# Kernel tuning notes

Measured on AMD Instinct MI355X. Metric: run time of the kernel, lower is better.

## Reference

```python
import jax, jax.numpy as jnp
import numpy as np

N_NODES = 50000
N_EDGES = 800000
IN_DIM = 128
HID_DIM = 256
N_CLASS = 40
PROP_STEP = 3
DROPOUT = 0.0  # eval-mode drop_node scale = (1 - DROPOUT)


def setup_inputs() -> dict:
    key = jax.random.key(0)
    k = jax.random.split(key, 6)
    features = jax.random.normal(k[0], (N_NODES, IN_DIM), dtype=jnp.float32)
    src = jax.random.randint(k[1], (N_EDGES,), 0, N_NODES)
    dst = jax.random.randint(k[2], (N_EDGES,), 0, N_NODES)
    W1 = jax.random.normal(k[3], (IN_DIM, HID_DIM), dtype=jnp.float32) / np.sqrt(IN_DIM)
    b1 = jnp.zeros((HID_DIM,), dtype=jnp.float32)
    W2 = jax.random.normal(k[4], (HID_DIM, N_CLASS), dtype=jnp.float32) / np.sqrt(HID_DIM)
    b2 = jnp.zeros((N_CLASS,), dtype=jnp.float32)
    return {"features": features, "src": src, "dst": dst,
            "W1": W1, "b1": b1, "W2": W2, "b2": b2}


def reference(features, src, dst, W1, b1, W2, b2):
    N = features.shape[0]
    # in-degree-based symmetric normalization: norm = deg^{-1/2}, deg clamped to >= 1
    degs = jax.ops.segment_sum(jnp.ones_like(dst, dtype=jnp.float32), dst,
                               num_segments=N)
    norm = jnp.clip(degs, 1.0, None) ** -0.5              # [N]
    w = norm[src] * norm[dst]                             # [E] edge weights (u_mul_v)

    # eval-mode drop_node: scale features by (1 - drop_rate)
    x = features * (1.0 - DROPOUT)
    y = x
    for _ in range(PROP_STEP):
        # u_mul_e: gather source features, scale by edge weight, scatter-sum to dst
        m = x[src] * w[:, None]                           # [E, F]
        x = jax.ops.segment_sum(m, dst, num_segments=N)   # [N, F]
        y = y + x
    feat = y / (PROP_STEP + 1)

    # MLP (use_bn=False, dropouts are 0 / eval): relu(linear) -> linear
    h = jax.nn.relu(feat @ W1 + b1)
    logits = h @ W2 + b2
    return jax.nn.log_softmax(logits, axis=-1)
```

## Files before the change

kernel.cpp:

```cpp
#include <hip/hip_runtime.h>

#define IN_DIM 128
#define HID    256
#define NCLS   40
#define BSHIFT 8
#define BSZ    256
#define MAXNB  256
#define CHUNK  4096
#define CAP    5120

static inline size_t align256(size_t x) { return (x + 255) & ~(size_t)255; }

typedef __attribute__((ext_vector_type(2))) float f32x2;

__device__ inline unsigned pack_bf16x2(float x, float y) {
    unsigned xb = __float_as_uint(x), yb = __float_as_uint(y);
    unsigned lo = (xb + 0x7fffu + ((xb >> 16) & 1u)) >> 16;
    unsigned hi = (yb + 0x7fffu + ((yb >> 16) & 1u)) >> 16;
    return lo | (hi << 16);
}
__device__ inline unsigned short f2bf(float x) {
    unsigned b = __float_as_uint(x);
    return (unsigned short)((b + 0x7fffu + ((b >> 16) & 1u)) >> 16);
}

__device__ inline unsigned pack_fp8x4(float a, float b, float c, float d) {
    int v = __builtin_amdgcn_cvt_pk_fp8_f32(a, b, 0, false);
    v = __builtin_amdgcn_cvt_pk_fp8_f32(c, d, v, true);
    return (unsigned)v;
}

__global__ __launch_bounds__(256) void init_cursor_kernel(int* __restrict__ cursor) {
    cursor[threadIdx.x] = threadIdx.x * CAP;
}

__global__ __launch_bounds__(256) void bucket_scatter_kernel(
        const int* __restrict__ src, const int* __restrict__ dst,
        int* __restrict__ bucketCursor, int2* __restrict__ ebuf, int E) {
    __shared__ int hist[MAXNB], lofs[MAXNB], lcur[MAXNB], gbase[MAXNB];
    __shared__ int2 bin[CHUNK];
    int t = threadIdx.x, lane = t & 63, wave = t >> 6;
    int start = blockIdx.x * CHUNK;
    int cnt = min(CHUNK, E - start);
    hist[t] = 0;
    __syncthreads();
    for (int i = t; i < cnt; i += 256) atomicAdd(&hist[dst[start + i] >> BSHIFT], 1);
    __syncthreads();
    int v = hist[t];
    int s = v;
    for (int off = 1; off < 64; off <<= 1) {
        int u = __shfl_up(s, off, 64);
        if (lane >= off) s += u;
    }
    __shared__ int wsum[4];
    if (lane == 63) wsum[wave] = s;
    __syncthreads();
    if (t == 0) {
        int c = 0;
        for (int i = 0; i < 4; ++i) { int x = wsum[i]; wsum[i] = c; c += x; }
    }
    __syncthreads();
    int excl = wsum[wave] + s - v;
    lofs[t] = excl; lcur[t] = excl;
    if (v) gbase[t] = atomicAdd(&bucketCursor[t], v);
    __syncthreads();
    for (int i = t; i < cnt; i += 256) {
        int s0 = src[start + i], d0 = dst[start + i];
        int r = atomicAdd(&lcur[d0 >> BSHIFT], 1);
        bin[r] = make_int2(s0, d0);
    }
    __syncthreads();
    for (int i = t; i < cnt; i += 256) {
        int2 e = bin[i];
        int b = e.y >> BSHIFT;
        ebuf[gbase[b] + i - lofs[b]] = e;
    }
}

__global__ __launch_bounds__(256) void build_norm_kernel(
        const int2* __restrict__ ebuf, const int* __restrict__ bucketCursor,
        int* __restrict__ offs, int* __restrict__ degs, float* __restrict__ norm, int N) {
    __shared__ int hist[BSZ];
    __shared__ int wsum[4];
    int b = blockIdx.x, t = threadIdx.x, lane = t & 63, wave = t >> 6;
    int base = b * CAP;
    int cnt = bucketCursor[b] - base;
    hist[t] = 0;
    __syncthreads();
    for (int i = t; i < cnt; i += 256) atomicAdd(&hist[ebuf[base + i].y & (BSZ - 1)], 1);
    __syncthreads();
    int v = hist[t];
    int s = v;
    for (int off = 1; off < 64; off <<= 1) {
        int u = __shfl_up(s, off, 64);
        if (lane >= off) s += u;
    }
    if (lane == 63) wsum[wave] = s;
    __syncthreads();
    if (t == 0) {
        int c = 0;
        for (int i = 0; i < 4; ++i) { int x = wsum[i]; wsum[i] = c; c += x; }
    }
    __syncthreads();
    int excl = wsum[wave] + s - v;
    int node = b * BSZ + t;
    if (node < N) {
        offs[node] = base + excl;
        degs[node] = v;
        norm[node] = rsqrtf((float)(v > 0 ? v : 1));
    }
}

__global__ __launch_bounds__(256) void build_csr_kernel(
        const int2* __restrict__ ebuf, const int* __restrict__ bucketCursor,
        const int* __restrict__ offs, const float* __restrict__ norm,
        int2* __restrict__ csr, int N) {
    __shared__ int lcur[BSZ];
    __shared__ float snorm[BSZ];
    int b = blockIdx.x, t = threadIdx.x;
    int base = b * CAP;
    int cnt = bucketCursor[b] - base;
    int node = b * BSZ + t;
    lcur[t] = (node < N) ? offs[node] : 0;
    snorm[t] = (node < N) ? norm[node] : 0.f;
    __syncthreads();
    for (int i = t; i < cnt; i += 256) {
        int2 e = ebuf[base + i];
        int li = e.y & (BSZ - 1);
        float w = norm[e.x] * snorm[li];
        int p = atomicAdd(&lcur[li], 1);
        csr[p] = make_int2(e.x, __float_as_int(w));
    }
}

__global__ void prep_kernel(const float* __restrict__ feat, unsigned* __restrict__ x0,
                            const float* __restrict__ W1, const float* __restrict__ W2,
                            unsigned short* __restrict__ W1T, unsigned short* __restrict__ W2T,
                            int nfeat_dw) {
    int i = blockIdx.x * blockDim.x + threadIdx.x;
    if (i < nfeat_dw) {
        float4 f = *(const float4*)(feat + (size_t)i * 4);
        x0[i] = pack_fp8x4(f.x, f.y, f.z, f.w);
        return;
    }
    int j = i - nfeat_dw;
    if (j < 256 * 128) {
        int n = j >> 7, k = j & 127;
        W1T[j] = f2bf(W1[k * 256 + n]);
        return;
    }
    int k2 = j - 256 * 128;
    if (k2 < 48 * 256) {
        int c = k2 >> 8, kk = k2 & 255;
        W2T[k2] = (c < 40) ? f2bf(W2[kk * 40 + c]) : (unsigned short)0;
    }
}

#define ACCP16(dd, ww)                                                        \
    {                                                                         \
        f32x2 wv2 = {(ww), (ww)};                                             \
        c0 += __builtin_amdgcn_cvt_pk_f32_fp8((int)(dd).x, false) * wv2;      \
        c1 += __builtin_amdgcn_cvt_pk_f32_fp8((int)(dd).x, true ) * wv2;      \
        c2 += __builtin_amdgcn_cvt_pk_f32_fp8((int)(dd).y, false) * wv2;      \
        c3 += __builtin_amdgcn_cvt_pk_f32_fp8((int)(dd).y, true ) * wv2;      \
        c4 += __builtin_amdgcn_cvt_pk_f32_fp8((int)(dd).z, false) * wv2;      \
        c5 += __builtin_amdgcn_cvt_pk_f32_fp8((int)(dd).z, true ) * wv2;      \
        c6 += __builtin_amdgcn_cvt_pk_f32_fp8((int)(dd).w, false) * wv2;      \
        c7 += __builtin_amdgcn_cvt_pk_f32_fp8((int)(dd).w, true ) * wv2;      \
    }

#define RED2(a) { a += __shfl_xor(a, 8, 64); a += __shfl_xor(a, 16, 64); }

__global__ __launch_bounds__(256) void prop_kernel(
        const unsigned* __restrict__ xin, unsigned* __restrict__ xout,
        const int* __restrict__ offs, const int* __restrict__ degs,
        const int2* __restrict__ csr, int N) {
    int t = threadIdx.x;
    int wv = t >> 6, lane = t & 63;
    int h = lane >> 5, hl = lane & 31;
    int g = hl >> 3, gl = hl & 7;
    int v = blockIdx.x * 8 + wv * 2 + h;
    if (v >= N) return;
    __shared__ int2 sIW[4][2][32];
    int start = offs[v], end = start + degs[v];
    f32x2 c0 = {0.f,0.f}, c1 = {0.f,0.f}, c2 = {0.f,0.f}, c3 = {0.f,0.f};
    f32x2 c4 = {0.f,0.f}, c5 = {0.f,0.f}, c6 = {0.f,0.f}, c7 = {0.f,0.f};
    for (int k = start; k < end; k += 32) {
        int cnt = min(32, end - k);
        if (hl < cnt) sIW[wv][h][hl] = csr[k + hl];
        int j = 0;
        for (; j + 16 <= cnt; j += 16) {
            uint4 d[4]; float w[4];
#pragma unroll
            for (int u = 0; u < 4; ++u) {
                int2 e = sIW[wv][h][j + 4 * u + g];
                w[u] = __int_as_float(e.y);
                d[u] = *(const uint4*)(xin + (size_t)e.x * 32 + gl * 4);
            }
#pragma unroll
            for (int u = 0; u < 4; ++u) ACCP16(d[u], w[u]);
        }
        int rem = cnt - j;
        if (rem > 8) {
            uint4 d[4]; float w[4];
#pragma unroll
            for (int u = 0; u < 4; ++u) {
                int idx = j + 4 * u + g;
                int2 e = sIW[wv][h][min(idx, cnt - 1)];
                w[u] = (idx < cnt) ? __int_as_float(e.y) : 0.f;
                d[u] = *(const uint4*)(xin + (size_t)e.x * 32 + gl * 4);
            }
#pragma unroll
            for (int u = 0; u < 4; ++u) ACCP16(d[u], w[u]);
        } else if (rem > 0) {
            uint4 d[2]; float w[2];
#pragma unroll
            for (int u = 0; u < 2; ++u) {
                int idx = j + 4 * u + g;
                int2 e = sIW[wv][h][min(idx, cnt - 1)];
                w[u] = (idx < cnt) ? __int_as_float(e.y) : 0.f;
                d[u] = *(const uint4*)(xin + (size_t)e.x * 32 + gl * 4);
            }
#pragma unroll
            for (int u = 0; u < 2; ++u) ACCP16(d[u], w[u]);
        }
    }
    float a0 = c0.x, a1 = c0.y, a2 = c1.x, a3 = c1.y;
    float a4 = c2.x, a5 = c2.y, a6 = c3.x, a7 = c3.y;
    float a8 = c4.x, a9 = c4.y, a10 = c5.x, a11 = c5.y;
    float a12 = c6.x, a13 = c6.y, a14 = c7.x, a15 = c7.y;
    RED2(a0); RED2(a1); RED2(a2); RED2(a3); RED2(a4); RED2(a5); RED2(a6); RED2(a7);
    RED2(a8); RED2(a9); RED2(a10); RED2(a11); RED2(a12); RED2(a13); RED2(a14); RED2(a15);
    if (g == 0) {
        uint4 o;
        o.x = pack_fp8x4(a0, a1, a2, a3);
        o.y = pack_fp8x4(a4, a5, a6, a7);
        o.z = pack_fp8x4(a8, a9, a10, a11);
        o.w = pack_fp8x4(a12, a13, a14, a15);
        *(uint4*)(xout + (size_t)v * 32 + gl * 4) = o;
    }
}

typedef __attribute__((ext_vector_type(8))) short bf16x8;
typedef __attribute__((ext_vector_type(4))) float f32x4;

#define SA_STRIDE 136
#define SH_STRIDE 264

__device__ inline void unpack8(uint2 u, float* q) {
    f32x2 p;
    p = __builtin_amdgcn_cvt_pk_f32_fp8((int)u.x, false); q[0] = p.x; q[1] = p.y;
    p = __builtin_amdgcn_cvt_pk_f32_fp8((int)u.x, true ); q[2] = p.x; q[3] = p.y;
    p = __builtin_amdgcn_cvt_pk_f32_fp8((int)u.y, false); q[4] = p.x; q[5] = p.y;
    p = __builtin_amdgcn_cvt_pk_f32_fp8((int)u.y, true ); q[6] = p.x; q[7] = p.y;
}

__global__ __launch_bounds__(256) void mlp16_kernel(
        const unsigned* __restrict__ x0, const unsigned* __restrict__ x1,
        const unsigned* __restrict__ x2, const unsigned* __restrict__ x3,
        const unsigned short* __restrict__ W1T, const float* __restrict__ b1,
        const unsigned short* __restrict__ W2T, const float* __restrict__ b2,
        float* __restrict__ out, int N) {
    __shared__ unsigned short sA[16 * SA_STRIDE];
    __shared__ unsigned short sH[16 * SH_STRIDE];
    __shared__ float sLog[16][49];
    int t = threadIdx.x, wv = t >> 6, lane = t & 63;
    int l15 = lane & 15, lq = lane >> 4;
    int base = blockIdx.x * 16;

    {
        int n = t >> 4, sg = t & 15;
        int gv = base + n;
        uint4 o = make_uint4(0u, 0u, 0u, 0u);
        if (gv < N) {
            size_t xo = (size_t)gv * 32 + sg * 2;
            uint2 u0 = *(const uint2*)(x0 + xo);
            uint2 u1 = *(const uint2*)(x1 + xo);
            uint2 u2 = *(const uint2*)(x2 + xo);
            uint2 u3 = *(const uint2*)(x3 + xo);
            float q0[8], q1[8], q2[8], q3[8];
            unpack8(u0, q0); unpack8(u1, q1); unpack8(u2, q2); unpack8(u3, q3);
            float s[8];
#pragma unroll
            for (int i = 0; i < 8; ++i) s[i] = (q0[i] + q1[i] + q2[i] + q3[i]) * 0.25f;
            o.x = pack_bf16x2(s[0], s[1]); o.y = pack_bf16x2(s[2], s[3]);
            o.z = pack_bf16x2(s[4], s[5]); o.w = pack_bf16x2(s[6], s[7]);
        }
        *(uint4*)&sA[n * SA_STRIDE + sg * 8] = o;
    }
    __syncthreads();

    f32x4 acc[4];
#pragma unroll
    for (int ht = 0; ht < 4; ++ht) acc[ht] = (f32x4){0.f, 0.f, 0.f, 0.f};
#pragma unroll
    for (int s = 0; s < 4; ++s) {
        bf16x8 afr = *(const bf16x8*)&sA[l15 * SA_STRIDE + s * 32 + lq * 8];
#pragma unroll
        for (int ht = 0; ht < 4; ++ht) {
            bf16x8 bfr = *(const bf16x8*)(W1T + ((wv * 64 + ht * 16 + l15) * 128 + s * 32 + lq * 8));
            acc[ht] = __builtin_amdgcn_mfma_f32_16x16x32_bf16(afr, bfr, acc[ht], 0, 0, 0);
        }
    }
#pragma unroll
    for (int ht = 0; ht < 4; ++ht) {
        int hid = wv * 64 + ht * 16 + l15;
        float bb = b1[hid];
#pragma unroll
        for (int r = 0; r < 4; ++r) {
            int node = lq * 4 + r;
            sH[node * SH_STRIDE + hid] = f2bf(fmaxf(acc[ht][r] + bb, 0.f));
        }
    }
    __syncthreads();

    if (wv < 3) {
        int ct = wv;
        f32x4 acc2 = (f32x4){0.f, 0.f, 0.f, 0.f};
#pragma unroll
        for (int s = 0; s < 8; ++s) {
            bf16x8 afr = *(const bf16x8*)&sH[l15 * SH_STRIDE + s * 32 + lq * 8];
            bf16x8 bfr = *(const bf16x8*)(W2T + ((ct * 16 + l15) * 256 + s * 32 + lq * 8));
            acc2 = __builtin_amdgcn_mfma_f32_16x16x32_bf16(afr, bfr, acc2, 0, 0, 0);
        }
        int c = ct * 16 + l15;
        float bb = (c < NCLS) ? b2[c] : 0.f;
#pragma unroll
        for (int r = 0; r < 4; ++r) sLog[lq * 4 + r][c] = acc2[r] + bb;
    }
    __syncthreads();
    if (wv != 0) return;

    float lg[3][4];
#pragma unroll
    for (int ct = 0; ct < 3; ++ct)
#pragma unroll
        for (int r = 0; r < 4; ++r) lg[ct][r] = sLog[lq * 4 + r][ct * 16 + l15];
#pragma unroll
    for (int r = 0; r < 4; ++r) {
        float m = fmaxf(lg[0][r], lg[1][r]);
        if (l15 < 8) m = fmaxf(m, lg[2][r]);
        for (int off = 1; off < 16; off <<= 1) m = fmaxf(m, __shfl_xor(m, off, 64));
        float ssum = __expf(lg[0][r] - m) + __expf(lg[1][r] - m) +
                     ((l15 < 8) ? __expf(lg[2][r] - m) : 0.f);
        for (int off = 1; off < 16; off <<= 1) ssum += __shfl_xor(ssum, off, 64);
        float ls = m + __logf(ssum);
        int node = base + lq * 4 + r;
        if (node < N) {
#pragma unroll
            for (int ct = 0; ct < 3; ++ct) {
                int c = ct * 16 + l15;
                if (c < NCLS) out[(size_t)node * NCLS + c] = lg[ct][r] - ls;
            }
        }
    }
}

extern "C" void kernel_launch(void* const* d_in, const int* in_sizes, int n_in,
                              void* d_out, int out_size, void* d_ws, size_t ws_size,
                              hipStream_t stream) {
    const float* feat = (const float*)d_in[0];
    const int*   src  = (const int*)d_in[1];
    const int*   dst  = (const int*)d_in[2];
    const float* W1   = (const float*)d_in[3];
    const float* b1   = (const float*)d_in[4];
    const float* W2   = (const float*)d_in[5];
    const float* b2   = (const float*)d_in[6];
    float* out = (float*)d_out;

    int N = in_sizes[0] / IN_DIM;
    int E = in_sizes[1];
    int NB = (N + BSZ - 1) / BSZ;

    char* ws = (char*)d_ws;
    size_t off = 0;
    float* norm   = (float*)(ws + off); off += align256((size_t)N * 4);
    int*   offs   = (int*)(ws + off);   off += align256((size_t)(N + 1) * 4);
    int*   degs   = (int*)(ws + off);   off += align256((size_t)N * 4);
    int*   bCur   = (int*)(ws + off);   off += align256((size_t)MAXNB * 4);
    int2*  csr    = (int2*)(ws + off);  off += align256((size_t)MAXNB * CAP * 8);
    int2*  ebuf   = (int2*)(ws + off);  off += align256((size_t)MAXNB * CAP * 8);
    unsigned* x0  = (unsigned*)(ws + off); off += align256((size_t)N * 32 * 4);
    unsigned* x1  = (unsigned*)(ws + off); off += align256((size_t)N * 32 * 4);
    unsigned* x2  = (unsigned*)(ws + off); off += align256((size_t)N * 32 * 4);
    unsigned* x3  = (unsigned*)(ws + off); off += align256((size_t)N * 32 * 4);
    unsigned short* W1T = (unsigned short*)(ws + off); off += align256((size_t)256 * 128 * 2);
    unsigned short* W2T = (unsigned short*)(ws + off); off += align256((size_t)48 * 256 * 2);
    (void)ws_size;

    init_cursor_kernel<<<1, 256, 0, stream>>>(bCur);

    int echunks = (E + CHUNK - 1) / CHUNK;
    bucket_scatter_kernel<<<echunks, 256, 0, stream>>>(src, dst, bCur, ebuf, E);
    build_norm_kernel<<<NB, 256, 0, stream>>>(ebuf, bCur, offs, degs, norm, N);
    build_csr_kernel<<<NB, 256, 0, stream>>>(ebuf, bCur, offs, norm, csr, N);

    int nprep = N * 32 + 256 * 128 + 48 * 256;
    prep_kernel<<<(nprep + 255) / 256, 256, 0, stream>>>(feat, x0, W1, W2, W1T, W2T, N * 32);

    int pb = (N + 7) / 8;
    prop_kernel<<<pb, 256, 0, stream>>>(x0, x1, offs, degs, csr, N);
    prop_kernel<<<pb, 256, 0, stream>>>(x1, x2, offs, degs, csr, N);
    prop_kernel<<<pb, 256, 0, stream>>>(x2, x3, offs, degs, csr, N);

    mlp16_kernel<<<(N + 15) / 16, 256, 0, stream>>>(x0, x1, x2, x3,
                                                    W1T, b1, W2T, b2, out, N);
}
```

Before: 213.4 us.

## Fold edge weights into node scaling and build CSR via global atomics

The per-edge normalization weight is removed from the CSR. The propagated features are instead kept in a scaled domain: the input is pre-multiplied by norm, each output by norm squared, and the MLP undoes the scaling with sqrt(deg). The CSR now stores only source indices (4 bytes per edge instead of 8), and prop no longer stages edges through shared memory. The bucketed CSR build is replaced by global atomic degree counting, a per-bucket scan and atomic placement, which adds heavy global atomic contention. Scaling the fp8 values may also change quantization error.

```diff
diff --git a/kernel.cpp b/kernel.cpp
--- a/kernel.cpp
+++ b/kernel.cpp
@@ -6,7 +6,6 @@
 #define BSHIFT 8
 #define BSZ    256
 #define MAXNB  256
-#define CHUNK  4096
 #define CAP    5120
 
 static inline size_t align256(size_t x) { return (x + 255) & ~(size_t)255; }
@@ -30,29 +29,40 @@
     return (unsigned)v;
 }
 
-__global__ __launch_bounds__(256) void init_cursor_kernel(int* __restrict__ cursor) {
-    cursor[threadIdx.x] = threadIdx.x * CAP;
-}
-
-__global__ __launch_bounds__(256) void bucket_scatter_kernel(
-        const int* __restrict__ src, const int* __restrict__ dst,
-        int* __restrict__ bucketCursor, int2* __restrict__ ebuf, int E) {
-    __shared__ int hist[MAXNB], lofs[MAXNB], lcur[MAXNB], gbase[MAXNB];
-    __shared__ int2 bin[CHUNK];
-    int t = threadIdx.x, lane = t & 63, wave = t >> 6;
-    int start = blockIdx.x * CHUNK;
-    int cnt = min(CHUNK, E - start);
-    hist[t] = 0;
-    __syncthreads();
-    for (int i = t; i < cnt; i += 256) atomicAdd(&hist[dst[start + i] >> BSHIFT], 1);
-    __syncthreads();
-    int v = hist[t];
+__global__ __launch_bounds__(256) void init_kernel(
+        int* __restrict__ degs,
+        const float* __restrict__ W1, const float* __restrict__ W2,
+        unsigned short* __restrict__ W1T, unsigned short* __restrict__ W2T, int N) {
+    int i = blockIdx.x * 256 + threadIdx.x;
+    if (i < N) degs[i] = 0;
+    if (i < 256 * 128) {
+        int n = i >> 7, k = i & 127;
+        W1T[i] = f2bf(W1[k * 256 + n]);
+    }
+    if (i < 48 * 256) {
+        int c = i >> 8, kk = i & 255;
+        W2T[i] = (c < 40) ? f2bf(W2[kk * 40 + c]) : (unsigned short)0;
+    }
+}
+
+__global__ __launch_bounds__(256) void deg_kernel(
+        const int* __restrict__ dst, int* __restrict__ degs, int E) {
+    int i = blockIdx.x * 256 + threadIdx.x;
+    if (i < E) atomicAdd(&degs[dst[i]], 1);
+}
+
+__global__ __launch_bounds__(256) void scan_kernel(
+        const int* __restrict__ degs, int* __restrict__ offs, int* __restrict__ cur,
+        float* __restrict__ norm, float* __restrict__ sqn, int N) {
+    __shared__ int wsum[4];
+    int b = blockIdx.x, t = threadIdx.x, lane = t & 63, wave = t >> 6;
+    int node = b * BSZ + t;
+    int v = (node < N) ? degs[node] : 0;
     int s = v;
     for (int off = 1; off < 64; off <<= 1) {
         int u = __shfl_up(s, off, 64);
         if (lane >= off) s += u;
     }
-    __shared__ int wsum[4];
     if (lane == 63) wsum[wave] = s;
     __syncthreads();
     if (t == 0) {
@@ -61,99 +71,35 @@
     }
     __syncthreads();
     int excl = wsum[wave] + s - v;
-    lofs[t] = excl; lcur[t] = excl;
-    if (v) gbase[t] = atomicAdd(&bucketCursor[t], v);
-    __syncthreads();
-    for (int i = t; i < cnt; i += 256) {
-        int s0 = src[start + i], d0 = dst[start + i];
-        int r = atomicAdd(&lcur[d0 >> BSHIFT], 1);
-        bin[r] = make_int2(s0, d0);
-    }
-    __syncthreads();
-    for (int i = t; i < cnt; i += 256) {
-        int2 e = bin[i];
-        int b = e.y >> BSHIFT;
-        ebuf[gbase[b] + i - lofs[b]] = e;
-    }
-}
-
-__global__ __launch_bounds__(256) void build_norm_kernel(
-        const int2* __restrict__ ebuf, const int* __restrict__ bucketCursor,
-        int* __restrict__ offs, int* __restrict__ degs, float* __restrict__ norm, int N) {
-    __shared__ int hist[BSZ];
-    __shared__ int wsum[4];
-    int b = blockIdx.x, t = threadIdx.x, lane = t & 63, wave = t >> 6;
-    int base = b * CAP;
-    int cnt = bucketCursor[b] - base;
-    hist[t] = 0;
-    __syncthreads();
-    for (int i = t; i < cnt; i += 256) atomicAdd(&hist[ebuf[base + i].y & (BSZ - 1)], 1);
-    __syncthreads();
-    int v = hist[t];
-    int s = v;
-    for (int off = 1; off < 64; off <<= 1) {
-        int u = __shfl_up(s, off, 64);
-        if (lane >= off) s += u;
-    }
-    if (lane == 63) wsum[wave] = s;
-    __syncthreads();
-    if (t == 0) {
-        int c = 0;
-        for (int i = 0; i < 4; ++i) { int x = wsum[i]; wsum[i] = c; c += x; }
-    }
-    __syncthreads();
-    int excl = wsum[wave] + s - v;
-    int node = b * BSZ + t;
     if (node < N) {
-        offs[node] = base + excl;
-        degs[node] = v;
-        norm[node] = rsqrtf((float)(v > 0 ? v : 1));
-    }
-}
-
-__global__ __launch_bounds__(256) void build_csr_kernel(
-        const int2* __restrict__ ebuf, const int* __restrict__ bucketCursor,
-        const int* __restrict__ offs, const float* __restrict__ norm,
-        int2* __restrict__ csr, int N) {
-    __shared__ int lcur[BSZ];
-    __shared__ float snorm[BSZ];
-    int b = blockIdx.x, t = threadIdx.x;
-    int base = b * CAP;
-    int cnt = bucketCursor[b] - base;
-    int node = b * BSZ + t;
-    lcur[t] = (node < N) ? offs[node] : 0;
-    snorm[t] = (node < N) ? norm[node] : 0.f;
-    __syncthreads();
-    for (int i = t; i < cnt; i += 256) {
-        int2 e = ebuf[base + i];
-        int li = e.y & (BSZ - 1);
-        float w = norm[e.x] * snorm[li];
-        int p = atomicAdd(&lcur[li], 1);
-        csr[p] = make_int2(e.x, __float_as_int(w));
-    }
-}
-
-__global__ void prep_kernel(const float* __restrict__ feat, unsigned* __restrict__ x0,
-                            const float* __restrict__ W1, const float* __restrict__ W2,
-                            unsigned short* __restrict__ W1T, unsigned short* __restrict__ W2T,
-                            int nfeat_dw) {
-    int i = blockIdx.x * blockDim.x + threadIdx.x;
-    if (i < nfeat_dw) {
-        float4 f = *(const float4*)(feat + (size_t)i * 4);
-        x0[i] = pack_fp8x4(f.x, f.y, f.z, f.w);
-        return;
-    }
-    int j = i - nfeat_dw;
-    if (j < 256 * 128) {
-        int n = j >> 7, k = j & 127;
-        W1T[j] = f2bf(W1[k * 256 + n]);
-        return;
-    }
-    int k2 = j - 256 * 128;
-    if (k2 < 48 * 256) {
-        int c = k2 >> 8, kk = k2 & 255;
-        W2T[k2] = (c < 40) ? f2bf(W2[kk * 40 + c]) : (unsigned short)0;
-    }
+        int o = b * CAP + excl;
+        offs[node] = o;
+        cur[node] = o;
+        float dc = (float)(v > 0 ? v : 1);
+        norm[node] = rsqrtf(dc);
+        sqn[node] = sqrtf(dc);
+    }
+}
+
+__global__ __launch_bounds__(256) void place_kernel(
+        const int* __restrict__ src, const int* __restrict__ dst,
+        int* __restrict__ cur, int* __restrict__ csrS, int E) {
+    int i = blockIdx.x * 256 + threadIdx.x;
+    if (i < E) {
+        int d = dst[i];
+        int p = atomicAdd(&cur[d], 1);
+        csrS[p] = src[i];
+    }
+}
+
+__global__ __launch_bounds__(256) void prep_kernel(
+        const float* __restrict__ feat, const float* __restrict__ norm,
+        unsigned* __restrict__ x0, int nfeat_dw) {
+    int i = blockIdx.x * 256 + threadIdx.x;
+    if (i >= nfeat_dw) return;
+    float s = norm[i >> 5];
+    float4 f = *(const float4*)(feat + (size_t)i * 4);
+    x0[i] = pack_fp8x4(f.x * s, f.y * s, f.z * s, f.w * s);
 }
 
 #define ACCP16(dd, ww)                                                        \
@@ -174,52 +120,46 @@
 __global__ __launch_bounds__(256) void prop_kernel(
         const unsigned* __restrict__ xin, unsigned* __restrict__ xout,
         const int* __restrict__ offs, const int* __restrict__ degs,
-        const int2* __restrict__ csr, int N) {
+        const float* __restrict__ norm, const int* __restrict__ csrS, int N) {
     int t = threadIdx.x;
     int wv = t >> 6, lane = t & 63;
     int h = lane >> 5, hl = lane & 31;
     int g = hl >> 3, gl = hl & 7;
     int v = blockIdx.x * 8 + wv * 2 + h;
     if (v >= N) return;
-    __shared__ int2 sIW[4][2][32];
     int start = offs[v], end = start + degs[v];
     f32x2 c0 = {0.f,0.f}, c1 = {0.f,0.f}, c2 = {0.f,0.f}, c3 = {0.f,0.f};
     f32x2 c4 = {0.f,0.f}, c5 = {0.f,0.f}, c6 = {0.f,0.f}, c7 = {0.f,0.f};
-    for (int k = start; k < end; k += 32) {
-        int cnt = min(32, end - k);
-        if (hl < cnt) sIW[wv][h][hl] = csr[k + hl];
-        int j = 0;
-        for (; j + 16 <= cnt; j += 16) {
+    for (int k = start; k < end; k += 16) {
+        int cnt = min(16, end - k);
+        if (cnt == 16) {
+            uint4 d[4];
+#pragma unroll
+            for (int u = 0; u < 4; ++u) {
+                int sx = csrS[k + 4 * u + g];
+                d[u] = *(const uint4*)(xin + (size_t)sx * 32 + gl * 4);
+            }
+#pragma unroll
+            for (int u = 0; u < 4; ++u) ACCP16(d[u], 1.0f);
+        } else if (cnt > 8) {
             uint4 d[4]; float w[4];
 #pragma unroll
             for (int u = 0; u < 4; ++u) {
-                int2 e = sIW[wv][h][j + 4 * u + g];
-                w[u] = __int_as_float(e.y);
-                d[u] = *(const uint4*)(xin + (size_t)e.x * 32 + gl * 4);
+                int il = 4 * u + g;
+                int sx = csrS[k + min(il, cnt - 1)];
+                w[u] = (il < cnt) ? 1.f : 0.f;
+                d[u] = *(const uint4*)(xin + (size_t)sx * 32 + gl * 4);
             }
 #pragma unroll
             for (int u = 0; u < 4; ++u) ACCP16(d[u], w[u]);
-        }
-        int rem = cnt - j;
-        if (rem > 8) {
-            uint4 d[4]; float w[4];
-#pragma unroll
-            for (int u = 0; u < 4; ++u) {
-                int idx = j + 4 * u + g;
-                int2 e = sIW[wv][h][min(idx, cnt - 1)];
-                w[u] = (idx < cnt) ? __int_as_float(e.y) : 0.f;
-                d[u] = *(const uint4*)(xin + (size_t)e.x * 32 + gl * 4);
-            }
-#pragma unroll
-            for (int u = 0; u < 4; ++u) ACCP16(d[u], w[u]);
-        } else if (rem > 0) {
+        } else {
             uint4 d[2]; float w[2];
 #pragma unroll
             for (int u = 0; u < 2; ++u) {
-                int idx = j + 4 * u + g;
-                int2 e = sIW[wv][h][min(idx, cnt - 1)];
-                w[u] = (idx < cnt) ? __int_as_float(e.y) : 0.f;
-                d[u] = *(const uint4*)(xin + (size_t)e.x * 32 + gl * 4);
+                int il = 4 * u + g;
+                int sx = csrS[k + min(il, cnt - 1)];
+                w[u] = (il < cnt) ? 1.f : 0.f;
+                d[u] = *(const uint4*)(xin + (size_t)sx * 32 + gl * 4);
             }
 #pragma unroll
             for (int u = 0; u < 2; ++u) ACCP16(d[u], w[u]);
@@ -232,11 +172,13 @@
     RED2(a0); RED2(a1); RED2(a2); RED2(a3); RED2(a4); RED2(a5); RED2(a6); RED2(a7);
     RED2(a8); RED2(a9); RED2(a10); RED2(a11); RED2(a12); RED2(a13); RED2(a14); RED2(a15);
     if (g == 0) {
+        float nv = norm[v];
+        float s2 = nv * nv;
         uint4 o;
-        o.x = pack_fp8x4(a0, a1, a2, a3);
-        o.y = pack_fp8x4(a4, a5, a6, a7);
-        o.z = pack_fp8x4(a8, a9, a10, a11);
-        o.w = pack_fp8x4(a12, a13, a14, a15);
+        o.x = pack_fp8x4(a0 * s2, a1 * s2, a2 * s2, a3 * s2);
+        o.y = pack_fp8x4(a4 * s2, a5 * s2, a6 * s2, a7 * s2);
+        o.z = pack_fp8x4(a8 * s2, a9 * s2, a10 * s2, a11 * s2);
+        o.w = pack_fp8x4(a12 * s2, a13 * s2, a14 * s2, a15 * s2);
         *(uint4*)(xout + (size_t)v * 32 + gl * 4) = o;
     }
 }
@@ -258,6 +200,7 @@
 __global__ __launch_bounds__(256) void mlp16_kernel(
         const unsigned* __restrict__ x0, const unsigned* __restrict__ x1,
         const unsigned* __restrict__ x2, const unsigned* __restrict__ x3,
+        const float* __restrict__ sqn,
         const unsigned short* __restrict__ W1T, const float* __restrict__ b1,
         const unsigned short* __restrict__ W2T, const float* __restrict__ b2,
         float* __restrict__ out, int N) {
@@ -280,9 +223,10 @@
             uint2 u3 = *(const uint2*)(x3 + xo);
             float q0[8], q1[8], q2[8], q3[8];
             unpack8(u0, q0); unpack8(u1, q1); unpack8(u2, q2); unpack8(u3, q3);
+            float fac = 0.25f * sqn[gv];
             float s[8];
 #pragma unroll
-            for (int i = 0; i < 8; ++i) s[i] = (q0[i] + q1[i] + q2[i] + q3[i]) * 0.25f;
+            for (int i = 0; i < 8; ++i) s[i] = (q0[i] + q1[i] + q2[i] + q3[i]) * fac;
             o.x = pack_bf16x2(s[0], s[1]); o.y = pack_bf16x2(s[2], s[3]);
             o.z = pack_bf16x2(s[4], s[5]); o.w = pack_bf16x2(s[6], s[7]);
         }
@@ -375,11 +319,11 @@
     char* ws = (char*)d_ws;
     size_t off = 0;
     float* norm   = (float*)(ws + off); off += align256((size_t)N * 4);
-    int*   offs   = (int*)(ws + off);   off += align256((size_t)(N + 1) * 4);
+    float* sqn    = (float*)(ws + off); off += align256((size_t)N * 4);
+    int*   offs   = (int*)(ws + off);   off += align256((size_t)N * 4);
     int*   degs   = (int*)(ws + off);   off += align256((size_t)N * 4);
-    int*   bCur   = (int*)(ws + off);   off += align256((size_t)MAXNB * 4);
-    int2*  csr    = (int2*)(ws + off);  off += align256((size_t)MAXNB * CAP * 8);
-    int2*  ebuf   = (int2*)(ws + off);  off += align256((size_t)MAXNB * CAP * 8);
+    int*   cur    = (int*)(ws + off);   off += align256((size_t)N * 4);
+    int*   csrS   = (int*)(ws + off);   off += align256((size_t)MAXNB * CAP * 4);
     unsigned* x0  = (unsigned*)(ws + off); off += align256((size_t)N * 32 * 4);
     unsigned* x1  = (unsigned*)(ws + off); off += align256((size_t)N * 32 * 4);
     unsigned* x2  = (unsigned*)(ws + off); off += align256((size_t)N * 32 * 4);
@@ -388,21 +332,19 @@
     unsigned short* W2T = (unsigned short*)(ws + off); off += align256((size_t)48 * 256 * 2);
     (void)ws_size;
 
-    init_cursor_kernel<<<1, 256, 0, stream>>>(bCur);
-
-    int echunks = (E + CHUNK - 1) / CHUNK;
-    bucket_scatter_kernel<<<echunks, 256, 0, stream>>>(src, dst, bCur, ebuf, E);
-    build_norm_kernel<<<NB, 256, 0, stream>>>(ebuf, bCur, offs, degs, norm, N);
-    build_csr_kernel<<<NB, 256, 0, stream>>>(ebuf, bCur, offs, norm, csr, N);
-
-    int nprep = N * 32 + 256 * 128 + 48 * 256;
-    prep_kernel<<<(nprep + 255) / 256, 256, 0, stream>>>(feat, x0, W1, W2, W1T, W2T, N * 32);
+    int nInit = N > 256 * 128 ? N : 256 * 128;
+    init_kernel<<<(nInit + 255) / 256, 256, 0, stream>>>(degs, W1, W2, W1T, W2T, N);
+    deg_kernel<<<(E + 255) / 256, 256, 0, stream>>>(dst, degs, E);
+    scan_kernel<<<NB, 256, 0, stream>>>(degs, offs, cur, norm, sqn, N);
+    place_kernel<<<(E + 255) / 256, 256, 0, stream>>>(src, dst, cur, csrS, E);
+
+    prep_kernel<<<(N * 32 + 255) / 256, 256, 0, stream>>>(feat, norm, x0, N * 32);
 
     int pb = (N + 7) / 8;
-    prop_kernel<<<pb, 256, 0, stream>>>(x0, x1, offs, degs, csr, N);
-    prop_kernel<<<pb, 256, 0, stream>>>(x1, x2, offs, degs, csr, N);
-    prop_kernel<<<pb, 256, 0, stream>>>(x2, x3, offs, degs, csr, N);
-
-    mlp16_kernel<<<(N + 15) / 16, 256, 0, stream>>>(x0, x1, x2, x3,
+    prop_kernel<<<pb, 256, 0, stream>>>(x0, x1, offs, degs, norm, csrS, N);
+    prop_kernel<<<pb, 256, 0, stream>>>(x1, x2, offs, degs, norm, csrS, N);
+    prop_kernel<<<pb, 256, 0, stream>>>(x2, x3, offs, degs, norm, csrS, N);
+
+    mlp16_kernel<<<(N + 15) / 16, 256, 0, stream>>>(x0, x1, x2, x3, sqn,
                                                     W1T, b1, W2T, b2, out, N);
 }
```

Result: slower. 292.8 us (+37.2%).
